# Kernel optimization log

Hardware: AMD Instinct MI355X
Metric: run time of the kernel (lower is better)

The kernel has to match this reference:

```python
import jax, jax.numpy as jnp
import numpy as np

B, N, H, TD = 64, 100, 128, 128
EPS = 1e-5  # BatchNorm eps (torch default)


def _xavier(k, shape):
    fan_in, fan_out = shape
    lim = (6.0 / (fan_in + fan_out)) ** 0.5
    return jax.random.uniform(k, shape, jnp.float32, -lim, lim)


def setup_inputs() -> dict:
    key = jax.random.key(0)
    ks = jax.random.split(key, 12)
    inp = {}
    inp["X"] = jax.random.randint(ks[0], (B, N * N), 0, 2).astype(jnp.float32)
    inp["time"] = jax.random.uniform(ks[1], (B,), jnp.float32)
    # Time_embedding MLP: Linear(TD->H), ReLU, Linear(H->H)
    inp["Wt1"] = _xavier(ks[2], (TD, H)); inp["bt1"] = jnp.zeros((H,), jnp.float32)
    inp["Wt2"] = _xavier(ks[3], (H, H)); inp["bt2"] = jnp.zeros((H,), jnp.float32)
    # TemporalGCNBlock.time_emb: Linear(H->N) + BN(N) + ReLU
    inp["Wtn"] = _xavier(ks[4], (H, N)); inp["btn"] = jnp.zeros((N,), jnp.float32)
    inp["g_tn"] = jnp.ones((N,), jnp.float32); inp["b_tn"] = jnp.zeros((N,), jnp.float32)
    # three GCNConv layers + BN
    inp["Wg1"] = _xavier(ks[5], (2 * N, H)); inp["bg1"] = jnp.zeros((H,), jnp.float32)
    inp["g1"] = jnp.ones((H,), jnp.float32); inp["bb1"] = jnp.zeros((H,), jnp.float32)
    inp["Wg2"] = _xavier(ks[6], (H, H)); inp["bg2"] = jnp.zeros((H,), jnp.float32)
    inp["g2"] = jnp.ones((H,), jnp.float32); inp["bb2"] = jnp.zeros((H,), jnp.float32)
    inp["Wg3"] = _xavier(ks[7], (H, H)); inp["bg3"] = jnp.zeros((H,), jnp.float32)
    inp["g3"] = jnp.ones((H,), jnp.float32); inp["bb3"] = jnp.zeros((H,), jnp.float32)
    # edge head: Linear(2H->H)+BN(H), Linear(2H->1)+BN(1)
    inp["We0"] = _xavier(ks[8], (2 * H, H)); inp["be0"] = jnp.zeros((H,), jnp.float32)
    inp["g_e0"] = jnp.ones((H,), jnp.float32); inp["b_e0"] = jnp.zeros((H,), jnp.float32)
    inp["We1"] = _xavier(ks[9], (2 * H, 1)); inp["be1"] = jnp.zeros((1,), jnp.float32)
    inp["g_e1"] = jnp.ones((1,), jnp.float32); inp["b_e1"] = jnp.zeros((1,), jnp.float32)
    return inp


def _bn(x, g, b):
    # eval-mode BatchNorm with fresh running stats (mean=0, var=1)
    return g * (x / jnp.sqrt(1.0 + EPS)) + b


def _timestep_embedding(t, dim, max_positions=10000):
    half = dim // 2
    freqs = jnp.exp(jnp.arange(half, dtype=jnp.float32) * (-np.log(max_positions) / (half - 1)))
    ang = t[:, None] * freqs[None, :]  # (B, half)
    return jnp.concatenate([jnp.sin(ang), jnp.cos(ang)], axis=1)


def reference(X, time, Wt1, bt1, Wt2, bt2, Wtn, btn, g_tn, b_tn,
              Wg1, bg1, g1, bb1, Wg2, bg2, g2, bb2, Wg3, bg3, g3, bb3,
              We0, be0, g_e0, b_e0, We1, be1, g_e1, b_e1):
    eye = jnp.eye(N, dtype=jnp.float32)
    # dense_to_sparse keeps nonzeros with unit edge weight; gcn_norm adds
    # remaining self-loops then symmetric-normalizes: A_hat = D^-1/2 (A|I) D^-1/2
    A = (X.reshape(B, N, N) != 0).astype(jnp.float32)
    At = jnp.maximum(A, eye)
    dinv = At.sum(-1) ** -0.5  # deg >= 1 thanks to self-loops
    Ah = dinv[:, :, None] * At * dinv[:, None, :]  # (B,N,N)

    # global time embedding (B,H)
    temb = _timestep_embedding(time, TD)
    h = jax.nn.relu(temb @ Wt1 + bt1) @ Wt2 + bt2
    # per-node time features (B,N); repeat_interleave == same vector per node
    t_node = jax.nn.relu(_bn(h @ Wtn + btn, g_tn, b_tn))
    x = jnp.concatenate([jnp.broadcast_to(eye, (B, N, N)),
                         jnp.broadcast_to(t_node[:, None, :], (B, N, N))], axis=-1)  # (B,N,2N)

    def gcn_block(x, W, b, g, bb):
        return jax.nn.relu(_bn(jnp.einsum('bij,bjh->bih', Ah, x @ W) + b, g, bb))

    x = gcn_block(x, Wg1, bg1, g1, bb1)
    x = gcn_block(x, Wg2, bg2, g2, bb2)
    x = gcn_block(x, Wg3, bg3, g3, bb3)  # (B,N,H)

    # edge head: Linear on concat(x_i, x_j) == split projections + broadcast add
    ei = x @ We0[:H]          # (B,N,H)
    ej = x @ We0[H:]          # (B,N,H)
    e0 = ei[:, :, None, :] + ej[:, None, :, :] + be0  # (B,N,N,H)
    e0 = _bn(e0, g_e0, b_e0)
    # Linear on concat(e0, time_emb): split into edge and time projections
    s = jnp.einsum('bijh,h->bij', e0, We1[:H, 0]) + (h @ We1[H:, 0])[:, None, None] + be1[0]
    s = _bn(s, g_e1[0], b_e1[0])
    out = (s * (1.0 - eye))[..., None]  # mask diagonal, (B,N,N,1)
    return out
```

## Files before the change

### kernel.cpp

```cpp
#include <hip/hip_runtime.h>
#include <math.h>

#define NB 64
#define NN 100
#define HH 128
#define HC 16
#define NCH 8

static constexpr float EPSBN = 1e-5f;

__global__ __launch_bounds__(256) void k_pre(
    const float* __restrict__ X, const float* __restrict__ timev,
    const float* __restrict__ Wt1, const float* __restrict__ bt1,
    const float* __restrict__ Wt2, const float* __restrict__ bt2,
    const float* __restrict__ Wtn, const float* __restrict__ btn,
    const float* __restrict__ g_tn, const float* __restrict__ b_tn,
    const float* __restrict__ Wg1, const float* __restrict__ We0,
    const float* __restrict__ We1, const float* __restrict__ be1,
    const float* __restrict__ be0, const float* __restrict__ g_e0,
    const float* __restrict__ b_e0,
    float* __restrict__ dinv, float* __restrict__ rs,
    float* __restrict__ u1, float* __restrict__ Dfull,
    float* __restrict__ vi, float* __restrict__ vj) {
    __shared__ float sX[NN * NN];
    __shared__ float sdinv[104];
    const int bx = blockIdx.x, t = threadIdx.x;
    const float rinv = 1.0f / sqrtf(1.f + EPSBN);

    if (bx < NB) {
        const int b = bx;
        float4* s4 = (float4*)sX;
        const float4* X4 = (const float4*)(X + b * NN * NN);
        for (int idx = t; idx < NN * NN / 4; idx += 256) s4[idx] = X4[idx];
        __syncthreads();
        if (t < 200) {
            const int row = t >> 1, h = t & 1;
            const float4* r4 = (const float4*)(sX + row * NN);
            float d = 0.f;
            const int qs = h ? 13 : 0, qe = h ? 25 : 13;
            for (int q = qs; q < qe; ++q) {
                float4 v = r4[q];
                d += v.x + v.y + v.z + v.w;
            }
            d += __shfl_xor(d, 1);
            if (h == 0) {
                if (sX[row * NN + row] == 0.f) d += 1.f;
                sdinv[row] = 1.0f / sqrtf(d);
            }
        }
        __syncthreads();
        if (t < 200) {
            const int row = t >> 1, h = t & 1;
            float ssum = 0.f;
            for (int j = h; j < NN; j += 2) {
                float x = sX[row * NN + j];
                float at = (row == j) ? 1.f : x;
                ssum += at * sdinv[j];
            }
            ssum += __shfl_xor(ssum, 1);
            if (h == 0) {
                rs[b * NN + row] = sdinv[row] * ssum;
                dinv[b * NN + row] = sdinv[row];
            }
        }
        return;
    }
    if (bx < 2 * NB) {
        const int b = bx - NB;
        float* s_temb = sX;
        float* s_h1 = sX + 128;
        float* s_h = sX + 256;
        float* s_tn = sX + 384;
        const float tt = timev[b];
        if (t < 128) {
            int k = t & 63;
            float f = expf((float)k * (-logf(10000.f) / 63.f));
            float a = tt * f;
            s_temb[t] = (t < 64) ? sinf(a) : cosf(a);
        }
        __syncthreads();
        if (t < 128) {
            float acc = bt1[t];
            for (int q = 0; q < HH; ++q) acc = fmaf(s_temb[q], Wt1[q * HH + t], acc);
            s_h1[t] = fmaxf(acc, 0.f);
        }
        __syncthreads();
        if (t < 128) {
            float acc = bt2[t];
            for (int q = 0; q < HH; ++q) acc = fmaf(s_h1[q], Wt2[q * HH + t], acc);
            s_h[t] = acc;
        }
        __syncthreads();
        if (t < NN) {
            float v = btn[t];
            for (int q = 0; q < HH; ++q) v = fmaf(s_h[q], Wtn[q * NN + t], v);
            s_tn[t] = fmaxf(fmaf(g_tn[t] * rinv, v, b_tn[t]), 0.f);
        }
        __syncthreads();
        if (t < 128) {
            float acc = 0.f;
            for (int n = 0; n < NN; ++n) acc = fmaf(s_tn[n], Wg1[(NN + n) * HH + t], acc);
            u1[b * HH + t] = acc;
        }
        if (t == 0) {
            float tp = 0.f;
            for (int q = 0; q < HH; ++q) tp = fmaf(s_h[q], We1[HH + q], tp);
            float K = 0.f;
            for (int hh = 0; hh < HH; ++hh)
                K += (be0[hh] * g_e0[hh] * rinv + b_e0[hh]) * We1[hh];
            Dfull[b] = tp + K + be1[0];
        }
        return;
    }
    if (t < 128) sX[t] = g_e0[t] * We1[t] * rinv;
    __syncthreads();
    if (t < 128) {
        float a = 0.f, cc = 0.f;
        for (int hh = 0; hh < HH; ++hh) {
            a = fmaf(We0[t * HH + hh], sX[hh], a);
            cc = fmaf(We0[(HH + t) * HH + hh], sX[hh], cc);
        }
        vi[t] = a;
        vj[t] = cc;
    }
}

__global__ __launch_bounds__(256, 2) void k_l1(
    const float* __restrict__ X, const float* __restrict__ dinv,
    const float* __restrict__ Wg1, const float* __restrict__ u1,
    const float* __restrict__ rs, const float* __restrict__ bg1,
    const float* __restrict__ g1, const float* __restrict__ bb1,
    float* __restrict__ out) {
    __shared__ float sZ[NN * 20];
    __shared__ float sdv[NN];
    const int b = blockIdx.x, hc = blockIdx.y * HC;
    const int t = threadIdx.x, jp = t & 3, ig = t >> 2;
    if (t < NN) sdv[t] = dinv[b * NN + t];
    __syncthreads();
    for (int idx = t; idx < 400; idx += 256) {
        int j = idx >> 2, c4 = idx & 3;
        float4 w = *(const float4*)&Wg1[j * HH + hc + c4 * 4];
        float dj = sdv[j];
        *(float4*)&sZ[j * 20 + c4 * 4] = make_float4(dj * w.x, dj * w.y, dj * w.z, dj * w.w);
    }
    __syncthreads();
    const int r0 = ig, r1 = (ig < 36) ? 64 + ig : ig;
    float a0[16], a1[16];
#pragma unroll
    for (int c = 0; c < 16; ++c) { a0[c] = 0.f; a1[c] = 0.f; }
    const float* __restrict__ Xb = X + b * NN * NN;
    const int j0 = jp * 28;
#pragma unroll
    for (int s = 0; s < 7; ++s) {
        const int j = j0 + s * 4;
        if (j < NN) {
            float4 v0 = *(const float4*)&Xb[r0 * NN + j];
            float4 v1 = *(const float4*)&Xb[r1 * NN + j];
#pragma unroll
            for (int jj = 0; jj < 4; ++jj) {
                const float e0 = (&v0.x)[jj], e1 = (&v1.x)[jj];
                const int zr = (j + jj) * 20;
#pragma unroll
                for (int c4 = 0; c4 < 4; ++c4) {
                    float4 z = *(const float4*)&sZ[zr + c4 * 4];
                    a0[c4 * 4 + 0] = fmaf(e0, z.x, a0[c4 * 4 + 0]);
                    a0[c4 * 4 + 1] = fmaf(e0, z.y, a0[c4 * 4 + 1]);
                    a0[c4 * 4 + 2] = fmaf(e0, z.z, a0[c4 * 4 + 2]);
                    a0[c4 * 4 + 3] = fmaf(e0, z.w, a0[c4 * 4 + 3]);
                    a1[c4 * 4 + 0] = fmaf(e1, z.x, a1[c4 * 4 + 0]);
                    a1[c4 * 4 + 1] = fmaf(e1, z.y, a1[c4 * 4 + 1]);
                    a1[c4 * 4 + 2] = fmaf(e1, z.z, a1[c4 * 4 + 2]);
                    a1[c4 * 4 + 3] = fmaf(e1, z.w, a1[c4 * 4 + 3]);
                }
            }
        }
    }
#pragma unroll
    for (int c = 0; c < 16; ++c) {
        a0[c] += __shfl_xor(a0[c], 1); a0[c] += __shfl_xor(a0[c], 2);
        a1[c] += __shfl_xor(a1[c], 1); a1[c] += __shfl_xor(a1[c], 2);
    }
    if (jp == 0) {
        const float rinv = 1.0f / sqrtf(1.f + EPSBN);
        const float di0 = sdv[r0], di1 = sdv[r1];
        const float cr0 = 1.f - Xb[r0 * NN + r0];
        const float cr1 = 1.f - Xb[r1 * NN + r1];
        const float rs0 = rs[b * NN + r0], rs1 = rs[b * NN + r1];
        float* ob = out + b * NN * HH;
#pragma unroll
        for (int c4 = 0; c4 < 4; ++c4) {
            float4 gv = *(const float4*)&g1[hc + c4 * 4];
            float4 bbv = *(const float4*)&bb1[hc + c4 * 4];
            float4 bgv = *(const float4*)&bg1[hc + c4 * 4];
            float4 uv = *(const float4*)&u1[b * HH + hc + c4 * 4];
            float4 y0, y1;
#pragma unroll
            for (int cc = 0; cc < 4; ++cc) {
                const int c = c4 * 4 + cc;
                float s0 = di0 * fmaf(cr0, sZ[r0 * 20 + c], a0[c]);
                float s1 = di1 * fmaf(cr1, sZ[r1 * 20 + c], a1[c]);
                (&y0.x)[cc] = fmaxf(fmaf((&gv.x)[cc] * rinv,
                                         s0 + rs0 * (&uv.x)[cc] + (&bgv.x)[cc],
                                         (&bbv.x)[cc]), 0.f);
                (&y1.x)[cc] = fmaxf(fmaf((&gv.x)[cc] * rinv,
                                         s1 + rs1 * (&uv.x)[cc] + (&bgv.x)[cc],
                                         (&bbv.x)[cc]), 0.f);
            }
            *(float4*)&ob[r0 * HH + hc + c4 * 4] = y0;
            if (ig < 36) *(float4*)&ob[r1 * HH + hc + c4 * 4] = y1;
        }
    }
}

template <bool LAST>
__global__ __launch_bounds__(256, 2) void k_layer(
    const float* __restrict__ X, const float* __restrict__ dinv,
    const float* __restrict__ xin, const float* __restrict__ W,
    const float* __restrict__ bg, const float* __restrict__ g,
    const float* __restrict__ bb, const float* __restrict__ vi,
    const float* __restrict__ vj, float* __restrict__ out,
    float* __restrict__ psi, float* __restrict__ psj) {
    __shared__ float sW[128 * 16];
    __shared__ float sZ[NN * 20];
    __shared__ float sdv[NN];
    const int b = blockIdx.x, hcb = blockIdx.y, hc = hcb * HC;
    const int t = threadIdx.x, jp = t & 3, ig = t >> 2;
    if (t < NN) sdv[t] = dinv[b * NN + t];
    for (int idx = t; idx < 512; idx += 256) {
        int k = idx >> 2, c4 = idx & 3;
        int kp = ((k & 31) << 2) | (k >> 5);
        *(float4*)&sW[kp * 16 + c4 * 4] = *(const float4*)&W[k * HH + hc + c4 * 4];
    }
    __syncthreads();
    const int r0 = ig, r1 = (ig < 36) ? 64 + ig : ig;
    const float* __restrict__ xb = xin + b * NN * HH;
    float a0[16], a1[16];
#pragma unroll
    for (int c = 0; c < 16; ++c) { a0[c] = 0.f; a1[c] = 0.f; }
    const int wb = jp << 4;
#pragma unroll
    for (int s = 0; s < 8; ++s) {
        const int k = (jp << 5) + s * 4;
        float4 x0 = *(const float4*)&xb[r0 * HH + k];
        float4 x1 = *(const float4*)&xb[r1 * HH + k];
#pragma unroll
        for (int kk = 0; kk < 4; ++kk) {
            const float e0 = (&x0.x)[kk], e1 = (&x1.x)[kk];
            const int wr = ((s * 4 + kk) << 6) + wb;
#pragma unroll
            for (int c4 = 0; c4 < 4; ++c4) {
                float4 w = *(const float4*)&sW[wr + c4 * 4];
                a0[c4 * 4 + 0] = fmaf(e0, w.x, a0[c4 * 4 + 0]);
                a0[c4 * 4 + 1] = fmaf(e0, w.y, a0[c4 * 4 + 1]);
                a0[c4 * 4 + 2] = fmaf(e0, w.z, a0[c4 * 4 + 2]);
                a0[c4 * 4 + 3] = fmaf(e0, w.w, a0[c4 * 4 + 3]);
                a1[c4 * 4 + 0] = fmaf(e1, w.x, a1[c4 * 4 + 0]);
                a1[c4 * 4 + 1] = fmaf(e1, w.y, a1[c4 * 4 + 1]);
                a1[c4 * 4 + 2] = fmaf(e1, w.z, a1[c4 * 4 + 2]);
                a1[c4 * 4 + 3] = fmaf(e1, w.w, a1[c4 * 4 + 3]);
            }
        }
    }
#pragma unroll
    for (int c = 0; c < 16; ++c) {
        a0[c] += __shfl_xor(a0[c], 1); a0[c] += __shfl_xor(a0[c], 2);
        a1[c] += __shfl_xor(a1[c], 1); a1[c] += __shfl_xor(a1[c], 2);
    }
    if (jp == 0) {
        const float di0 = sdv[r0], di1 = sdv[r1];
#pragma unroll
        for (int c4 = 0; c4 < 4; ++c4) {
            *(float4*)&sZ[r0 * 20 + c4 * 4] =
                make_float4(di0 * a0[c4 * 4 + 0], di0 * a0[c4 * 4 + 1],
                            di0 * a0[c4 * 4 + 2], di0 * a0[c4 * 4 + 3]);
            if (ig < 36)
                *(float4*)&sZ[r1 * 20 + c4 * 4] =
                    make_float4(di1 * a1[c4 * 4 + 0], di1 * a1[c4 * 4 + 1],
                                di1 * a1[c4 * 4 + 2], di1 * a1[c4 * 4 + 3]);
        }
    }
    __syncthreads();
#pragma unroll
    for (int c = 0; c < 16; ++c) { a0[c] = 0.f; a1[c] = 0.f; }
    const float* __restrict__ Xb = X + b * NN * NN;
    const int j0 = jp * 28;
#pragma unroll
    for (int s = 0; s < 7; ++s) {
        const int j = j0 + s * 4;
        if (j < NN) {
            float4 v0 = *(const float4*)&Xb[r0 * NN + j];
            float4 v1 = *(const float4*)&Xb[r1 * NN + j];
#pragma unroll
            for (int jj = 0; jj < 4; ++jj) {
                const float e0 = (&v0.x)[jj], e1 = (&v1.x)[jj];
                const int zr = (j + jj) * 20;
#pragma unroll
                for (int c4 = 0; c4 < 4; ++c4) {
                    float4 z = *(const float4*)&sZ[zr + c4 * 4];
                    a0[c4 * 4 + 0] = fmaf(e0, z.x, a0[c4 * 4 + 0]);
                    a0[c4 * 4 + 1] = fmaf(e0, z.y, a0[c4 * 4 + 1]);
                    a0[c4 * 4 + 2] = fmaf(e0, z.z, a0[c4 * 4 + 2]);
                    a0[c4 * 4 + 3] = fmaf(e0, z.w, a0[c4 * 4 + 3]);
                    a1[c4 * 4 + 0] = fmaf(e1, z.x, a1[c4 * 4 + 0]);
                    a1[c4 * 4 + 1] = fmaf(e1, z.y, a1[c4 * 4 + 1]);
                    a1[c4 * 4 + 2] = fmaf(e1, z.z, a1[c4 * 4 + 2]);
                    a1[c4 * 4 + 3] = fmaf(e1, z.w, a1[c4 * 4 + 3]);
                }
            }
        }
    }
#pragma unroll
    for (int c = 0; c < 16; ++c) {
        a0[c] += __shfl_xor(a0[c], 1); a0[c] += __shfl_xor(a0[c], 2);
        a1[c] += __shfl_xor(a1[c], 1); a1[c] += __shfl_xor(a1[c], 2);
    }
    if (jp == 0) {
        const float rinv = 1.0f / sqrtf(1.f + EPSBN);
        const float di0 = sdv[r0], di1 = sdv[r1];
        const float cr0 = 1.f - Xb[r0 * NN + r0];
        const float cr1 = 1.f - Xb[r1 * NN + r1];
        float y0[16], y1[16];
#pragma unroll
        for (int c4 = 0; c4 < 4; ++c4) {
            float4 gv = *(const float4*)&g[hc + c4 * 4];
            float4 bbv = *(const float4*)&bb[hc + c4 * 4];
            float4 bgv = *(const float4*)&bg[hc + c4 * 4];
#pragma unroll
            for (int cc = 0; cc < 4; ++cc) {
                const int c = c4 * 4 + cc;
                float s0 = di0 * fmaf(cr0, sZ[r0 * 20 + c], a0[c]);
                float s1 = di1 * fmaf(cr1, sZ[r1 * 20 + c], a1[c]);
                y0[c] = fmaxf(fmaf((&gv.x)[cc] * rinv, s0 + (&bgv.x)[cc], (&bbv.x)[cc]), 0.f);
                y1[c] = fmaxf(fmaf((&gv.x)[cc] * rinv, s1 + (&bgv.x)[cc], (&bbv.x)[cc]), 0.f);
            }
        }
        if (LAST) {
            float pi0 = 0.f, pj0 = 0.f, pi1 = 0.f, pj1 = 0.f;
#pragma unroll
            for (int c = 0; c < 16; ++c) {
                const float vic = vi[hc + c], vjc = vj[hc + c];
                pi0 = fmaf(y0[c], vic, pi0); pj0 = fmaf(y0[c], vjc, pj0);
                pi1 = fmaf(y1[c], vic, pi1); pj1 = fmaf(y1[c], vjc, pj1);
            }
            psi[(b * NN + r0) * NCH + hcb] = pi0;
            psj[(b * NN + r0) * NCH + hcb] = pj0;
            if (ig < 36) {
                psi[(b * NN + r1) * NCH + hcb] = pi1;
                psj[(b * NN + r1) * NCH + hcb] = pj1;
            }
        } else {
            float* ob = out + b * NN * HH;
#pragma unroll
            for (int c4 = 0; c4 < 4; ++c4) {
                *(float4*)&ob[r0 * HH + hc + c4 * 4] =
                    make_float4(y0[c4 * 4 + 0], y0[c4 * 4 + 1], y0[c4 * 4 + 2], y0[c4 * 4 + 3]);
                if (ig < 36)
                    *(float4*)&ob[r1 * HH + hc + c4 * 4] =
                        make_float4(y1[c4 * 4 + 0], y1[c4 * 4 + 1], y1[c4 * 4 + 2], y1[c4 * 4 + 3]);
            }
        }
    }
}

__global__ __launch_bounds__(256) void k_out(
    const float* __restrict__ psi, const float* __restrict__ psj,
    const float* __restrict__ Dfull, const float* __restrict__ g_e1,
    const float* __restrict__ b_e1, float* __restrict__ outp) {
    __shared__ float ssi[25], ssj[NN];
    const int b = blockIdx.x, i0 = blockIdx.y * 25;
    const int t = threadIdx.x;
    if (t < NN) {
        float s = 0.f;
        const float4* p = (const float4*)(psj + (b * NN + t) * NCH);
#pragma unroll
        for (int q = 0; q < NCH / 4; ++q) {
            float4 v = p[q];
            s += v.x + v.y + v.z + v.w;
        }
        ssj[t] = s;
    }
    if (t >= 128 && t < 128 + 25) {
        int i = t - 128;
        float s = 0.f;
        const float4* p = (const float4*)(psi + (b * NN + i0 + i) * NCH);
#pragma unroll
        for (int q = 0; q < NCH / 4; ++q) {
            float4 v = p[q];
            s += v.x + v.y + v.z + v.w;
        }
        ssi[i] = s;
    }
    __syncthreads();
    const float rinv = 1.0f / sqrtf(1.f + EPSBN);
    const float D = Dfull[b], ge = g_e1[0] * rinv, be = b_e1[0];
    float* ob = outp + b * NN * NN + i0 * NN;
    for (int e = t; e < 25 * NN; e += 256) {
        int ii = e / NN, j = e - ii * NN;
        float v = fmaf(ge, ssi[ii] + ssj[j] + D, be);
        ob[e] = (i0 + ii == j) ? 0.f : v;
    }
}

extern "C" void kernel_launch(void* const* d_in, const int* in_sizes, int n_in,
                              void* d_out, int out_size, void* d_ws, size_t ws_size,
                              hipStream_t stream) {
    const float* X    = (const float*)d_in[0];
    const float* timev= (const float*)d_in[1];
    const float* Wt1  = (const float*)d_in[2];
    const float* bt1  = (const float*)d_in[3];
    const float* Wt2  = (const float*)d_in[4];
    const float* bt2  = (const float*)d_in[5];
    const float* Wtn  = (const float*)d_in[6];
    const float* btn  = (const float*)d_in[7];
    const float* g_tn = (const float*)d_in[8];
    const float* b_tn = (const float*)d_in[9];
    const float* Wg1  = (const float*)d_in[10];
    const float* bg1  = (const float*)d_in[11];
    const float* g1   = (const float*)d_in[12];
    const float* bb1  = (const float*)d_in[13];
    const float* Wg2  = (const float*)d_in[14];
    const float* bg2  = (const float*)d_in[15];
    const float* g2   = (const float*)d_in[16];
    const float* bb2  = (const float*)d_in[17];
    const float* Wg3  = (const float*)d_in[18];
    const float* bg3  = (const float*)d_in[19];
    const float* g3   = (const float*)d_in[20];
    const float* bb3  = (const float*)d_in[21];
    const float* We0  = (const float*)d_in[22];
    const float* be0  = (const float*)d_in[23];
    const float* g_e0 = (const float*)d_in[24];
    const float* b_e0 = (const float*)d_in[25];
    const float* We1  = (const float*)d_in[26];
    const float* be1  = (const float*)d_in[27];
    const float* g_e1 = (const float*)d_in[28];
    const float* b_e1 = (const float*)d_in[29];

    float* ws = (float*)d_ws;
    float* dinv  = ws;
    float* rs    = dinv + 6400;
    float* u1    = rs + 6400;
    float* Dfull = u1 + 8192;
    float* vi    = Dfull + 64;
    float* vj    = vi + 128;
    float* x1    = vj + 128;
    float* x2    = x1 + 819200;
    float* psi   = x1;
    float* psj   = x1 + 51200;

    k_pre<<<dim3(2 * NB + 1), dim3(256), 0, stream>>>(
        X, timev, Wt1, bt1, Wt2, bt2, Wtn, btn, g_tn, b_tn, Wg1, We0, We1, be1,
        be0, g_e0, b_e0, dinv, rs, u1, Dfull, vi, vj);

    k_l1<<<dim3(NB, NCH), dim3(256), 0, stream>>>(X, dinv, Wg1, u1, rs, bg1, g1, bb1, x1);
    k_layer<false><<<dim3(NB, NCH), dim3(256), 0, stream>>>(X, dinv, x1, Wg2, bg2, g2,
                                                            bb2, nullptr, nullptr, x2,
                                                            nullptr, nullptr);
    k_layer<true><<<dim3(NB, NCH), dim3(256), 0, stream>>>(X, dinv, x2, Wg3, bg3, g3,
                                                           bb3, vi, vj, nullptr, psi, psj);

    k_out<<<dim3(NB, 4), dim3(256), 0, stream>>>(psi, psj, Dfull, g_e1, b_e1,
                                                 (float*)d_out);
}
```

Measured before the change: 53.29 us.

## Fuse preprocessing into layer-1 and output head into last layer via atomic counter

Drops the separate preprocessing and output kernels. Each layer-1 block now recomputes the degree normalization, the time-embedding MLP and the u1 projection locally instead of reading them from a prior kernel. The last GCN layer computes its vi/vj slices itself, and the final block per batch (found with an atomic counter after a threadfence) writes the edge output. This cuts launches from five to three plus a memset, in exchange for redundant per-block MLP work across eight column blocks and a serial tail in the last block of each batch.

```diff
diff --git a/kernel.cpp b/kernel.cpp
--- a/kernel.cpp
+++ b/kernel.cpp
@@ -9,133 +9,95 @@
 
 static constexpr float EPSBN = 1e-5f;
 
-__global__ __launch_bounds__(256) void k_pre(
+__global__ __launch_bounds__(256, 2) void k_l1f(
     const float* __restrict__ X, const float* __restrict__ timev,
     const float* __restrict__ Wt1, const float* __restrict__ bt1,
     const float* __restrict__ Wt2, const float* __restrict__ bt2,
     const float* __restrict__ Wtn, const float* __restrict__ btn,
     const float* __restrict__ g_tn, const float* __restrict__ b_tn,
-    const float* __restrict__ Wg1, const float* __restrict__ We0,
+    const float* __restrict__ Wg1, const float* __restrict__ bg1,
+    const float* __restrict__ g1, const float* __restrict__ bb1,
     const float* __restrict__ We1, const float* __restrict__ be1,
     const float* __restrict__ be0, const float* __restrict__ g_e0,
     const float* __restrict__ b_e0,
-    float* __restrict__ dinv, float* __restrict__ rs,
-    float* __restrict__ u1, float* __restrict__ Dfull,
-    float* __restrict__ vi, float* __restrict__ vj) {
-    __shared__ float sX[NN * NN];
-    __shared__ float sdinv[104];
-    const int bx = blockIdx.x, t = threadIdx.x;
+    float* __restrict__ dinv, float* __restrict__ Dfull,
+    float* __restrict__ out) {
+    __shared__ float sZ[NN * 20];
+    __shared__ float sdv[104], srs[104], su1[128];
+    __shared__ float sml[512];
+    const int b = blockIdx.x, hcb = blockIdx.y, hc = hcb * HC;
+    const int t = threadIdx.x, jp = t & 3, ig = t >> 2;
     const float rinv = 1.0f / sqrtf(1.f + EPSBN);
-
-    if (bx < NB) {
-        const int b = bx;
-        float4* s4 = (float4*)sX;
-        const float4* X4 = (const float4*)(X + b * NN * NN);
-        for (int idx = t; idx < NN * NN / 4; idx += 256) s4[idx] = X4[idx];
-        __syncthreads();
-        if (t < 200) {
-            const int row = t >> 1, h = t & 1;
-            const float4* r4 = (const float4*)(sX + row * NN);
-            float d = 0.f;
-            const int qs = h ? 13 : 0, qe = h ? 25 : 13;
-            for (int q = qs; q < qe; ++q) {
-                float4 v = r4[q];
-                d += v.x + v.y + v.z + v.w;
-            }
-            d += __shfl_xor(d, 1);
-            if (h == 0) {
-                if (sX[row * NN + row] == 0.f) d += 1.f;
-                sdinv[row] = 1.0f / sqrtf(d);
-            }
-        }
-        __syncthreads();
-        if (t < 200) {
-            const int row = t >> 1, h = t & 1;
-            float ssum = 0.f;
-            for (int j = h; j < NN; j += 2) {
-                float x = sX[row * NN + j];
-                float at = (row == j) ? 1.f : x;
-                ssum += at * sdinv[j];
-            }
-            ssum += __shfl_xor(ssum, 1);
-            if (h == 0) {
-                rs[b * NN + row] = sdinv[row] * ssum;
-                dinv[b * NN + row] = sdinv[row];
-            }
-        }
-        return;
-    }
-    if (bx < 2 * NB) {
-        const int b = bx - NB;
-        float* s_temb = sX;
-        float* s_h1 = sX + 128;
-        float* s_h = sX + 256;
-        float* s_tn = sX + 384;
+    const float* __restrict__ Xb = X + b * NN * NN;
+
+    if (t < 200) {
+        const int row = t >> 1, h = t & 1;
+        const float4* r4 = (const float4*)(Xb + row * NN);
+        float d = 0.f;
+        const int qs = h ? 13 : 0, qe = h ? 25 : 13;
+        for (int q = qs; q < qe; ++q) {
+            float4 v = r4[q];
+            d += v.x + v.y + v.z + v.w;
+        }
+        d += __shfl_xor(d, 1);
+        if (h == 0) {
+            if (Xb[row * NN + row] == 0.f) d += 1.f;
+            sdv[row] = 1.0f / sqrtf(d);
+        }
+    }
+    {
         const float tt = timev[b];
         if (t < 128) {
             int k = t & 63;
             float f = expf((float)k * (-logf(10000.f) / 63.f));
             float a = tt * f;
-            s_temb[t] = (t < 64) ? sinf(a) : cosf(a);
+            sml[t] = (t < 64) ? sinf(a) : cosf(a);
         }
         __syncthreads();
         if (t < 128) {
             float acc = bt1[t];
-            for (int q = 0; q < HH; ++q) acc = fmaf(s_temb[q], Wt1[q * HH + t], acc);
-            s_h1[t] = fmaxf(acc, 0.f);
+            for (int q = 0; q < HH; ++q) acc = fmaf(sml[q], Wt1[q * HH + t], acc);
+            sml[128 + t] = fmaxf(acc, 0.f);
         }
         __syncthreads();
         if (t < 128) {
             float acc = bt2[t];
-            for (int q = 0; q < HH; ++q) acc = fmaf(s_h1[q], Wt2[q * HH + t], acc);
-            s_h[t] = acc;
+            for (int q = 0; q < HH; ++q) acc = fmaf(sml[128 + q], Wt2[q * HH + t], acc);
+            sml[256 + t] = acc;
         }
         __syncthreads();
         if (t < NN) {
             float v = btn[t];
-            for (int q = 0; q < HH; ++q) v = fmaf(s_h[q], Wtn[q * NN + t], v);
-            s_tn[t] = fmaxf(fmaf(g_tn[t] * rinv, v, b_tn[t]), 0.f);
+            for (int q = 0; q < HH; ++q) v = fmaf(sml[256 + q], Wtn[q * NN + t], v);
+            sml[384 + t] = fmaxf(fmaf(g_tn[t] * rinv, v, b_tn[t]), 0.f);
         }
         __syncthreads();
         if (t < 128) {
             float acc = 0.f;
-            for (int n = 0; n < NN; ++n) acc = fmaf(s_tn[n], Wg1[(NN + n) * HH + t], acc);
-            u1[b * HH + t] = acc;
-        }
-        if (t == 0) {
+            for (int n = 0; n < NN; ++n) acc = fmaf(sml[384 + n], Wg1[(NN + n) * HH + t], acc);
+            su1[t] = acc;
+        }
+        if (hcb == 0 && t == 0) {
             float tp = 0.f;
-            for (int q = 0; q < HH; ++q) tp = fmaf(s_h[q], We1[HH + q], tp);
+            for (int q = 0; q < HH; ++q) tp = fmaf(sml[256 + q], We1[HH + q], tp);
             float K = 0.f;
             for (int hh = 0; hh < HH; ++hh)
                 K += (be0[hh] * g_e0[hh] * rinv + b_e0[hh]) * We1[hh];
             Dfull[b] = tp + K + be1[0];
         }
-        return;
-    }
-    if (t < 128) sX[t] = g_e0[t] * We1[t] * rinv;
-    __syncthreads();
-    if (t < 128) {
-        float a = 0.f, cc = 0.f;
-        for (int hh = 0; hh < HH; ++hh) {
-            a = fmaf(We0[t * HH + hh], sX[hh], a);
-            cc = fmaf(We0[(HH + t) * HH + hh], sX[hh], cc);
-        }
-        vi[t] = a;
-        vj[t] = cc;
-    }
-}
-
-__global__ __launch_bounds__(256, 2) void k_l1(
-    const float* __restrict__ X, const float* __restrict__ dinv,
-    const float* __restrict__ Wg1, const float* __restrict__ u1,
-    const float* __restrict__ rs, const float* __restrict__ bg1,
-    const float* __restrict__ g1, const float* __restrict__ bb1,
-    float* __restrict__ out) {
-    __shared__ float sZ[NN * 20];
-    __shared__ float sdv[NN];
-    const int b = blockIdx.x, hc = blockIdx.y * HC;
-    const int t = threadIdx.x, jp = t & 3, ig = t >> 2;
-    if (t < NN) sdv[t] = dinv[b * NN + t];
+    }
+    if (t < 200) {
+        const int row = t >> 1, h = t & 1;
+        float ssum = 0.f;
+        for (int j = h; j < NN; j += 2) {
+            float x = Xb[row * NN + j];
+            float at = (row == j) ? 1.f : x;
+            ssum += at * sdv[j];
+        }
+        ssum += __shfl_xor(ssum, 1);
+        if (h == 0) srs[row] = sdv[row] * ssum;
+    }
+    if (hcb == 0 && t < NN) dinv[b * NN + t] = sdv[t];
     __syncthreads();
     for (int idx = t; idx < 400; idx += 256) {
         int j = idx >> 2, c4 = idx & 3;
@@ -148,7 +110,6 @@
     float a0[16], a1[16];
 #pragma unroll
     for (int c = 0; c < 16; ++c) { a0[c] = 0.f; a1[c] = 0.f; }
-    const float* __restrict__ Xb = X + b * NN * NN;
     const int j0 = jp * 28;
 #pragma unroll
     for (int s = 0; s < 7; ++s) {
@@ -181,18 +142,17 @@
         a1[c] += __shfl_xor(a1[c], 1); a1[c] += __shfl_xor(a1[c], 2);
     }
     if (jp == 0) {
-        const float rinv = 1.0f / sqrtf(1.f + EPSBN);
         const float di0 = sdv[r0], di1 = sdv[r1];
         const float cr0 = 1.f - Xb[r0 * NN + r0];
         const float cr1 = 1.f - Xb[r1 * NN + r1];
-        const float rs0 = rs[b * NN + r0], rs1 = rs[b * NN + r1];
+        const float rs0 = srs[r0], rs1 = srs[r1];
         float* ob = out + b * NN * HH;
 #pragma unroll
         for (int c4 = 0; c4 < 4; ++c4) {
             float4 gv = *(const float4*)&g1[hc + c4 * 4];
             float4 bbv = *(const float4*)&bb1[hc + c4 * 4];
             float4 bgv = *(const float4*)&bg1[hc + c4 * 4];
-            float4 uv = *(const float4*)&u1[b * HH + hc + c4 * 4];
+            float4 uv = *(const float4*)&su1[hc + c4 * 4];
             float4 y0, y1;
 #pragma unroll
             for (int cc = 0; cc < 4; ++cc) {
@@ -217,21 +177,36 @@
     const float* __restrict__ X, const float* __restrict__ dinv,
     const float* __restrict__ xin, const float* __restrict__ W,
     const float* __restrict__ bg, const float* __restrict__ g,
-    const float* __restrict__ bb, const float* __restrict__ vi,
-    const float* __restrict__ vj, float* __restrict__ out,
-    float* __restrict__ psi, float* __restrict__ psj) {
+    const float* __restrict__ bb,
+    const float* __restrict__ We0, const float* __restrict__ We1,
+    const float* __restrict__ g_e0,
+    const float* __restrict__ Dfull, const float* __restrict__ g_e1,
+    const float* __restrict__ b_e1,
+    float* __restrict__ out, float* __restrict__ psi, float* __restrict__ psj,
+    int* __restrict__ cnt, float* __restrict__ outp) {
     __shared__ float sW[128 * 16];
     __shared__ float sZ[NN * 20];
     __shared__ float sdv[NN];
+    __shared__ float sc[128], sVi[16], sVj[16];
+    __shared__ int sdone;
     const int b = blockIdx.x, hcb = blockIdx.y, hc = hcb * HC;
     const int t = threadIdx.x, jp = t & 3, ig = t >> 2;
+    const float rinv = 1.0f / sqrtf(1.f + EPSBN);
     if (t < NN) sdv[t] = dinv[b * NN + t];
+    if (LAST && t >= 112 && t < 240) sc[t - 112] = g_e0[t - 112] * We1[t - 112] * rinv;
     for (int idx = t; idx < 512; idx += 256) {
         int k = idx >> 2, c4 = idx & 3;
         int kp = ((k & 31) << 2) | (k >> 5);
         *(float4*)&sW[kp * 16 + c4 * 4] = *(const float4*)&W[k * HH + hc + c4 * 4];
     }
     __syncthreads();
+    if (LAST && t < 32) {
+        const int h = hc + (t & 15);
+        const float* row = We0 + ((t < 16) ? h : (HH + h)) * HH;
+        float a = 0.f;
+        for (int hh = 0; hh < HH; ++hh) a = fmaf(row[hh], sc[hh], a);
+        if (t < 16) sVi[t] = a; else sVj[t - 16] = a;
+    }
     const int r0 = ig, r1 = (ig < 36) ? 64 + ig : ig;
     const float* __restrict__ xb = xin + b * NN * HH;
     float a0[16], a1[16];
@@ -315,7 +290,6 @@
         a1[c] += __shfl_xor(a1[c], 1); a1[c] += __shfl_xor(a1[c], 2);
     }
     if (jp == 0) {
-        const float rinv = 1.0f / sqrtf(1.f + EPSBN);
         const float di0 = sdv[r0], di1 = sdv[r1];
         const float cr0 = 1.f - Xb[r0 * NN + r0];
         const float cr1 = 1.f - Xb[r1 * NN + r1];
@@ -338,9 +312,8 @@
             float pi0 = 0.f, pj0 = 0.f, pi1 = 0.f, pj1 = 0.f;
 #pragma unroll
             for (int c = 0; c < 16; ++c) {
-                const float vic = vi[hc + c], vjc = vj[hc + c];
-                pi0 = fmaf(y0[c], vic, pi0); pj0 = fmaf(y0[c], vjc, pj0);
-                pi1 = fmaf(y1[c], vic, pi1); pj1 = fmaf(y1[c], vjc, pj1);
+                pi0 = fmaf(y0[c], sVi[c], pi0); pj0 = fmaf(y0[c], sVj[c], pj0);
+                pi1 = fmaf(y1[c], sVi[c], pi1); pj1 = fmaf(y1[c], sVj[c], pj1);
             }
             psi[(b * NN + r0) * NCH + hcb] = pi0;
             psj[(b * NN + r0) * NCH + hcb] = pj0;
@@ -360,44 +333,40 @@
             }
         }
     }
-}
-
-__global__ __launch_bounds__(256) void k_out(
-    const float* __restrict__ psi, const float* __restrict__ psj,
-    const float* __restrict__ Dfull, const float* __restrict__ g_e1,
-    const float* __restrict__ b_e1, float* __restrict__ outp) {
-    __shared__ float ssi[25], ssj[NN];
-    const int b = blockIdx.x, i0 = blockIdx.y * 25;
-    const int t = threadIdx.x;
-    if (t < NN) {
-        float s = 0.f;
-        const float4* p = (const float4*)(psj + (b * NN + t) * NCH);
-#pragma unroll
-        for (int q = 0; q < NCH / 4; ++q) {
-            float4 v = p[q];
-            s += v.x + v.y + v.z + v.w;
-        }
-        ssj[t] = s;
-    }
-    if (t >= 128 && t < 128 + 25) {
-        int i = t - 128;
-        float s = 0.f;
-        const float4* p = (const float4*)(psi + (b * NN + i0 + i) * NCH);
-#pragma unroll
-        for (int q = 0; q < NCH / 4; ++q) {
-            float4 v = p[q];
-            s += v.x + v.y + v.z + v.w;
-        }
-        ssi[i] = s;
-    }
-    __syncthreads();
-    const float rinv = 1.0f / sqrtf(1.f + EPSBN);
-    const float D = Dfull[b], ge = g_e1[0] * rinv, be = b_e1[0];
-    float* ob = outp + b * NN * NN + i0 * NN;
-    for (int e = t; e < 25 * NN; e += 256) {
-        int ii = e / NN, j = e - ii * NN;
-        float v = fmaf(ge, ssi[ii] + ssj[j] + D, be);
-        ob[e] = (i0 + ii == j) ? 0.f : v;
+    if (LAST) {
+        __threadfence();
+        __syncthreads();
+        if (t == 0) sdone = atomicAdd(&cnt[b], 1);
+        __syncthreads();
+        if (sdone == NCH - 1) {
+            __threadfence();
+            float* ssj = sZ;
+            float* ssi = sZ + 128;
+            if (t < NN) {
+                const float4* p = (const float4*)(psj + (b * NN + t) * NCH);
+                float4 v0 = p[0], v1 = p[1];
+                ssj[t] = v0.x + v0.y + v0.z + v0.w + v1.x + v1.y + v1.z + v1.w;
+            }
+            if (t >= 128 && t < 128 + NN) {
+                int i = t - 128;
+                const float4* p = (const float4*)(psi + (b * NN + i) * NCH);
+                float4 v0 = p[0], v1 = p[1];
+                ssi[i] = v0.x + v0.y + v0.z + v0.w + v1.x + v1.y + v1.z + v1.w;
+            }
+            __syncthreads();
+            const float D = Dfull[b], ge = g_e1[0] * rinv, be = b_e1[0];
+            float4* ob4 = (float4*)(outp + b * NN * NN);
+            for (int e = t; e < NN * NN / 4; e += 256) {
+                const int i = e / 25, jj = (e - i * 25) * 4;
+                const float si = ssi[i];
+                float4 v;
+                v.x = (i == jj + 0) ? 0.f : fmaf(ge, si + ssj[jj + 0] + D, be);
+                v.y = (i == jj + 1) ? 0.f : fmaf(ge, si + ssj[jj + 1] + D, be);
+                v.z = (i == jj + 2) ? 0.f : fmaf(ge, si + ssj[jj + 2] + D, be);
+                v.w = (i == jj + 3) ? 0.f : fmaf(ge, si + ssj[jj + 3] + D, be);
+                ob4[e] = v;
+            }
+        }
     }
 }
 
@@ -436,28 +405,29 @@
     const float* b_e1 = (const float*)d_in[29];
 
     float* ws = (float*)d_ws;
-    float* dinv  = ws;
-    float* rs    = dinv + 6400;
-    float* u1    = rs + 6400;
-    float* Dfull = u1 + 8192;
-    float* vi    = Dfull + 64;
-    float* vj    = vi + 128;
-    float* x1    = vj + 128;
+    int*   cnt   = (int*)ws;
+    float* base  = ws + 64;
+    float* dinv  = base;
+    float* Dfull = dinv + 6400;
+    float* x1    = Dfull + 64;
     float* x2    = x1 + 819200;
     float* psi   = x1;
     float* psj   = x1 + 51200;
 
-    k_pre<<<dim3(2 * NB + 1), dim3(256), 0, stream>>>(
-        X, timev, Wt1, bt1, Wt2, bt2, Wtn, btn, g_tn, b_tn, Wg1, We0, We1, be1,
-        be0, g_e0, b_e0, dinv, rs, u1, Dfull, vi, vj);
-
-    k_l1<<<dim3(NB, NCH), dim3(256), 0, stream>>>(X, dinv, Wg1, u1, rs, bg1, g1, bb1, x1);
-    k_layer<false><<<dim3(NB, NCH), dim3(256), 0, stream>>>(X, dinv, x1, Wg2, bg2, g2,
-                                                            bb2, nullptr, nullptr, x2,
-                                                            nullptr, nullptr);
-    k_layer<true><<<dim3(NB, NCH), dim3(256), 0, stream>>>(X, dinv, x2, Wg3, bg3, g3,
-                                                           bb3, vi, vj, nullptr, psi, psj);
-
-    k_out<<<dim3(NB, 4), dim3(256), 0, stream>>>(psi, psj, Dfull, g_e1, b_e1,
-                                                 (float*)d_out);
+    hipMemsetAsync(cnt, 0, 256, stream);
+
+    k_l1f<<<dim3(NB, NCH), dim3(256), 0, stream>>>(
+        X, timev, Wt1, bt1, Wt2, bt2, Wtn, btn, g_tn, b_tn,
+        Wg1, bg1, g1, bb1, We1, be1, be0, g_e0, b_e0,
+        dinv, Dfull, x1);
+
+    k_layer<false><<<dim3(NB, NCH), dim3(256), 0, stream>>>(
+        X, dinv, x1, Wg2, bg2, g2, bb2,
+        nullptr, nullptr, nullptr, nullptr, nullptr, nullptr,
+        x2, nullptr, nullptr, nullptr, nullptr);
+
+    k_layer<true><<<dim3(NB, NCH), dim3(256), 0, stream>>>(
+        X, dinv, x2, Wg3, bg3, g3, bb3,
+        We0, We1, g_e0, Dfull, g_e1, b_e1,
+        nullptr, psi, psj, cnt, (float*)d_out);
 }
```

Result: slower. 114.6 us (+115.0%).
